# Kernel optimization log

Hardware: AMD Instinct MI355X
Metric: run time of the kernel (lower is better)

## Reference

```python
import jax, jax.numpy as jnp
import numpy as np

B, S, HID = 4, 2048, 2048
NH, NKV, HD = 16, 4, 128  # query heads, kv heads, head_dim


def setup_inputs() -> dict:
    key = jax.random.key(0)
    ks = jax.random.split(key, 7)
    scale = 1.0 / np.sqrt(HID)
    x = jax.random.normal(ks[0], (B, S, HID), dtype=jnp.float32)
    # rope tables (interleaved-pair convention matching rotate_half)
    inv_freq = 1.0 / (1000000.0 ** (np.arange(0, HD, 2, dtype=np.float32) / HD))
    t = np.arange(S, dtype=np.float32)
    freqs = np.outer(t, inv_freq)                      # (S, HD/2)
    emb = np.repeat(freqs, 2, axis=-1)                 # (S, HD) interleaved
    cos = jnp.asarray(np.cos(emb))
    sin = jnp.asarray(np.sin(emb))
    wq = jax.random.normal(ks[1], (HID, NH * HD), dtype=jnp.float32) * scale
    wk = jax.random.normal(ks[2], (HID, NKV * HD), dtype=jnp.float32) * scale
    wv = jax.random.normal(ks[3], (HID, NKV * HD), dtype=jnp.float32) * scale
    wo = jax.random.normal(ks[4], (NH * HD, HID), dtype=jnp.float32) * scale
    return {"x": x, "cos": cos, "sin": sin, "wq": wq, "wk": wk, "wv": wv, "wo": wo}


def _rotate_half(u):
    even = u[..., ::2]
    odd = u[..., 1::2]
    return jnp.stack((-odd, even), axis=-1).reshape(u.shape)


def reference(x, cos, sin, wq, wk, wv, wo):
    b, s, _ = x.shape
    rep = NH // NKV
    q = (x @ wq).reshape(b, s, NH, HD)
    k = (x @ wk).reshape(b, s, NKV, HD)
    v = (x @ wv).reshape(b, s, NKV, HD)
    # RoPE: cos/sin (S, HD) -> broadcast over batch and heads (unsqueeze_dim=1)
    c = cos[:s][None, :, None, :]
    sn = sin[:s][None, :, None, :]
    q = q * c + _rotate_half(q) * sn
    k = k * c + _rotate_half(k) * sn
    # GQA: group query heads per kv head; avoid materializing repeated K/V
    q = q.transpose(0, 2, 1, 3).reshape(b, NKV, rep, s, HD)   # (b, kv, rep, s, d)
    k = k.transpose(0, 2, 1, 3)                                # (b, kv, s, d)
    v = v.transpose(0, 2, 1, 3)                                # (b, kv, s, d)
    scores = jnp.einsum("bgrqd,bgkd->bgrqk", q, k) / jnp.sqrt(jnp.float32(HD))
    causal = jnp.tril(jnp.ones((s, s), dtype=bool))
    scores = jnp.where(causal, scores, jnp.finfo(scores.dtype).min)
    probs = jax.nn.softmax(scores, axis=-1)
    out = jnp.einsum("bgrqk,bgkd->bgrqd", probs, v)            # (b, kv, rep, s, d)
    out = out.reshape(b, NH, s, HD).transpose(0, 2, 1, 3).reshape(b, s, NH * HD)
    return out @ wo
```

## Files before the change

### kernel.cpp

```cpp
#include <hip/hip_runtime.h>

#define HIDD 2048
#define SEQ  2048
#define BATCH 4
#define NHQ  16
#define NKVH 4
#define HDIM 128
#define QKVN 3072

typedef unsigned short u16;
typedef unsigned int   u32;
using bf16x8 = __attribute__((ext_vector_type(8))) __bf16;
using u16x8  = __attribute__((ext_vector_type(8))) u16;
using u16x4  = __attribute__((ext_vector_type(4))) u16;
using f32x4  = __attribute__((ext_vector_type(4))) float;

__device__ __forceinline__ float bf2f(u16 v){ u32 u = ((u32)v) << 16; float f; __builtin_memcpy(&f, &u, 4); return f; }
__device__ __forceinline__ u16 f2bf(float f){ u32 u; __builtin_memcpy(&u, &f, 4); u += 0x7fffu + ((u >> 16) & 1u); return (u16)(u >> 16); }

__device__ __forceinline__ void gl_lds16(const void* g, void* l){
  __builtin_amdgcn_global_load_lds((const __attribute__((address_space(1))) void*)g,
                                   (__attribute__((address_space(3))) void*)l, 16, 0, 0);
}


__global__ void cvt_f32_bf16(const float* __restrict__ in, u16* __restrict__ out, int n4){
  int i = blockIdx.x * 256 + threadIdx.x;
  if (i >= n4) return;
  float4 v = ((const float4*)in)[i];
  u16x4 o; o[0] = f2bf(v.x); o[1] = f2bf(v.y); o[2] = f2bf(v.z); o[3] = f2bf(v.w);
  ((u16x4*)out)[i] = o;
}

__global__ void transpose_cvt_f32(const float* __restrict__ in, u16* __restrict__ out, int R, int C){
  __shared__ float t[32][33];
  int c0 = blockIdx.x * 32, r0 = blockIdx.y * 32;
  int tx = threadIdx.x, ty = threadIdx.y;
  #pragma unroll
  for (int i = 0; i < 4; i++)
    t[ty + 8*i][tx] = in[(size_t)(r0 + ty + 8*i) * C + c0 + tx];
  __syncthreads();
  #pragma unroll
  for (int i = 0; i < 4; i++)
    out[(size_t)(c0 + ty + 8*i) * R + r0 + tx] = f2bf(t[tx][ty + 8*i]);
}

__global__ void transpose_v(const u16* __restrict__ V, u16* __restrict__ Vt, int ld, int voff){
  __shared__ u16 t[32][33];
  int bg = blockIdx.z;
  int b = bg >> 2, g = bg & 3;
  const u16* in = V + (size_t)b * SEQ * ld + voff + g * HDIM;
  u16* out = Vt + (size_t)bg * HDIM * SEQ;
  int c0 = blockIdx.x * 32, r0 = blockIdx.y * 32;
  int tx = threadIdx.x, ty = threadIdx.y;
  #pragma unroll
  for (int i = 0; i < 4; i++)
    t[ty + 8*i][tx] = in[(size_t)(r0 + ty + 8*i) * ld + c0 + tx];
  __syncthreads();
  #pragma unroll
  for (int i = 0; i < 4; i++)
    out[(size_t)(c0 + ty + 8*i) * SEQ + r0 + tx] = t[tx][ty + 8*i];
}

__global__ void rope_kernel(u16* __restrict__ X, int ld, int ncl,
                            const float* __restrict__ ct, const float* __restrict__ st,
                            float scale, int n8){
  int i = blockIdx.x * 256 + threadIdx.x;
  if (i >= n8) return;
  int e0 = i * 8;
  int row = e0 >> ncl;
  int col = e0 & ((1 << ncl) - 1);
  int pos = row & (SEQ - 1);
  int dd  = col & (HDIM - 1);
  u16* p = X + (size_t)row * ld + col;
  u16x8 v = *(const u16x8*)p;
  const float* cp = ct + (size_t)pos * HDIM + dd;
  const float* sp = st + (size_t)pos * HDIM + dd;
  float f[8];
  #pragma unroll
  for (int j = 0; j < 8; j++) f[j] = bf2f(v[j]);
  u16x8 o;
  #pragma unroll
  for (int j = 0; j < 8; j += 2){
    float c = cp[j], s = sp[j];
    float e = f[j], od = f[j+1];
    o[j]   = f2bf((e * c - od * s) * scale);
    o[j+1] = f2bf((od * c + e * s) * scale);
  }
  *(u16x8*)p = o;
}

template<int OUT_BF16>
__global__ __launch_bounds__(256) void gemm_bt(const u16* __restrict__ A, const u16* __restrict__ Bt,
                                               void* __restrict__ Cv, int M, int N, int K){
  __shared__ __align__(16) u16 As[128*32];
  __shared__ __align__(16) u16 Bs[128*32];
  const int tid = threadIdx.x;
  const int wid = tid >> 6, lane = tid & 63;
  const int lr = lane & 15, lk = lane >> 4;
  const int m0 = blockIdx.y * 128, n0 = blockIdx.x * 128;
  const int wr = (wid >> 1) * 64, wc = (wid & 1) * 64;

  f32x4 acc[4][4];
  #pragma unroll
  for (int m = 0; m < 4; m++)
    #pragma unroll
    for (int n = 0; n < 4; n++) acc[m][n] = f32x4{0.f,0.f,0.f,0.f};

  const int srow = lane >> 2;
  const int swz  = ((lane & 3) * 8) ^ ((srow & 3) * 8);
  const u16* Ag = A  + (size_t)(m0 + wid*32 + srow) * K + swz;
  const u16* Bg = Bt + (size_t)(n0 + wid*32 + srow) * K + swz;
  u16* Asl = As + wid * 1024;
  u16* Bsl = Bs + wid * 1024;
  const int rsw = (lr & 3) * 8;

  for (int k0 = 0; k0 < K; k0 += 32){
    gl_lds16(Ag + k0,          Asl);
    gl_lds16(Ag + k0 + 16*K,   Asl + 512);
    gl_lds16(Bg + k0,          Bsl);
    gl_lds16(Bg + k0 + 16*K,   Bsl + 512);
    __syncthreads();
    bf16x8 a[4], b[4];
    #pragma unroll
    for (int m = 0; m < 4; m++) a[m] = *(const bf16x8*)&As[(wr + m*16 + lr)*32 + ((lk*8) ^ rsw)];
    #pragma unroll
    for (int n = 0; n < 4; n++) b[n] = *(const bf16x8*)&Bs[(wc + n*16 + lr)*32 + ((lk*8) ^ rsw)];
    #pragma unroll
    for (int m = 0; m < 4; m++)
      #pragma unroll
      for (int n = 0; n < 4; n++)
        acc[m][n] = __builtin_amdgcn_mfma_f32_16x16x32_bf16(a[m], b[n], acc[m][n], 0, 0, 0);
    __syncthreads();
  }
  #pragma unroll
  for (int m = 0; m < 4; m++)
    #pragma unroll
    for (int n = 0; n < 4; n++)
      #pragma unroll
      for (int i = 0; i < 4; i++){
        int gr = m0 + wr + m*16 + lk*4 + i;
        int gc = n0 + wc + n*16 + lr;
        float v = acc[m][n][i];
        if (OUT_BF16) ((u16*)Cv)[(size_t)gr * N + gc] = f2bf(v);
        else          ((float*)Cv)[(size_t)gr * N + gc] = v;
      }
}

__global__ __launch_bounds__(256) void attn_kernel(const u16* __restrict__ QKV, const u16* __restrict__ Vt,
                                                   u16* __restrict__ O){
  const int qt = (gridDim.x - 1) - blockIdx.x;
  const int h = blockIdx.y, b = blockIdx.z;
  const int g = h >> 2;
  const int tid = threadIdx.x;
  const int wid = tid >> 6, lane = tid & 63;
  const int lr = lane & 15, lk = lane >> 4;
  const int q0 = qt * 128;
  const int q0w = q0 + wid * 32;

  __shared__ __align__(16) u16 Ks[2][64*128];
  __shared__ __align__(16) u16 Vs[2][128*64];
  __shared__ __align__(16) u16 Ps[4][16*72];
  u16* Pw = &Ps[wid][0];

  bf16x8 qf[2][4];
  #pragma unroll
  for (int qh = 0; qh < 2; qh++){
    const u16* qp = QKV + (size_t)(b*SEQ + q0w + qh*16 + lr) * QKVN + h*HDIM + lk*8;
    #pragma unroll
    for (int c = 0; c < 4; c++) qf[qh][c] = *(const bf16x8*)(qp + c*32);
  }

  const int klr = lane >> 4, kj = lane & 15;
  const int vlr = lane >> 3, vj = lane & 7;
  const u16* Kst[4]; const u16* Vst[4];
  {
    const u16* Kbase = QKV + (size_t)b * SEQ * QKVN + HIDD + g*HDIM;
    const u16* Vbase = Vt + (size_t)(b*NKVH + g) * HDIM * SEQ;
    #pragma unroll
    for (int iw = 0; iw < 4; iw++){
      int kcb = wid*4 + iw;
      int r   = kcb*4 + klr;
      Kst[iw] = Kbase + (size_t)r * QKVN + ((kj ^ (r & 7)) << 3);
      int d   = kcb*8 + vlr;
      Vst[iw] = Vbase + (size_t)d * SEQ + ((vj ^ (d & 7)) << 3);
    }
  }

  f32x4 oacc[2][8];
  #pragma unroll
  for (int qh = 0; qh < 2; qh++)
    #pragma unroll
    for (int f = 0; f < 8; f++) oacc[qh][f] = f32x4{0.f,0.f,0.f,0.f};
  float m_i[2] = {-1e30f, -1e30f}, l_i[2] = {0.f, 0.f};

  const int nt = 2 * (qt + 1);
  int cur = 0;
  #pragma unroll
  for (int iw = 0; iw < 4; iw++){
    int kcb = wid*4 + iw;
    gl_lds16(Kst[iw], &Ks[0][kcb << 9]);
    gl_lds16(Vst[iw], &Vs[0][kcb << 9]);
    Kst[iw] += 64 * QKVN;
    Vst[iw] += 64;
  }

  for (int t = 0; t < nt; ++t){
    __syncthreads();
    if (t + 1 < nt){
      #pragma unroll
      for (int iw = 0; iw < 4; iw++){
        int kcb = wid*4 + iw;
        gl_lds16(Kst[iw], &Ks[cur ^ 1][kcb << 9]);
        gl_lds16(Vst[iw], &Vs[cur ^ 1][kcb << 9]);
        Kst[iw] += 64 * QKVN;
        Vst[iw] += 64;
      }
    }
    const int kv0 = t * 64;
    if (kv0 <= q0w + 31){
      f32x4 sf[2][4];
      #pragma unroll
      for (int n = 0; n < 4; n++){
        bf16x8 kf[4];
        #pragma unroll
        for (int c = 0; c < 4; c++)
          kf[c] = *(const bf16x8*)&Ks[cur][(n*16 + lr)*128 + (((c*4 + lk) ^ (lr & 7)) << 3)];
        #pragma unroll
        for (int qh = 0; qh < 2; qh++){
          f32x4 a = f32x4{0.f,0.f,0.f,0.f};
          #pragma unroll
          for (int c = 0; c < 4; c++)
            a = __builtin_amdgcn_mfma_f32_16x16x32_bf16(kf[c], qf[qh][c], a, 0, 0, 0);
          sf[qh][n] = a;
        }
      }
      if (kv0 + 63 > q0w){
        #pragma unroll
        for (int qh = 0; qh < 2; qh++)
          #pragma unroll
          for (int n = 0; n < 4; n++)
            #pragma unroll
            for (int i = 0; i < 4; i++){
              int kvg = kv0 + n*16 + lk*4 + i;
              int qg  = q0w + qh*16 + lr;
              if (kvg > qg) sf[qh][n][i] = -1e30f;
            }
      }
      #pragma unroll
      for (int qh = 0; qh < 2; qh++){
        float rm = sf[qh][0][0];
        #pragma unroll
        for (int n = 0; n < 4; n++)
          #pragma unroll
          for (int i = 0; i < 4; i++) rm = fmaxf(rm, sf[qh][n][i]);
        rm = fmaxf(rm, __shfl_xor(rm, 16));
        rm = fmaxf(rm, __shfl_xor(rm, 32));

        if (!__all(rm <= m_i[qh] + 11.5f)){
          float mn = fmaxf(m_i[qh], rm);
          float cf = exp2f(m_i[qh] - mn);
          m_i[qh] = mn; l_i[qh] *= cf;
          float cfq[4];
          #pragma unroll
          for (int i = 0; i < 4; i++) cfq[i] = __shfl(cf, lk*4 + i);
          #pragma unroll
          for (int f = 0; f < 8; f++)
            #pragma unroll
            for (int i = 0; i < 4; i++) oacc[qh][f][i] *= cfq[i];
        }
        float rs = 0.f;
        #pragma unroll
        for (int n = 0; n < 4; n++){
          u16x4 pp;
          #pragma unroll
          for (int i = 0; i < 4; i++){
            float pv = exp2f(sf[qh][n][i] - m_i[qh]);
            rs += pv;
            pp[i] = f2bf(pv);
          }
          *(u16x4*)&Pw[lr*72 + n*16 + lk*4] = pp;
        }
        rs += __shfl_xor(rs, 16);
        rs += __shfl_xor(rs, 32);
        l_i[qh] += rs;

        #pragma unroll
        for (int kc = 0; kc < 2; kc++){
          bf16x8 pf = *(const bf16x8*)&Pw[lr*72 + kc*32 + lk*8];
          #pragma unroll
          for (int f = 0; f < 8; f++){
            bf16x8 vf = *(const bf16x8*)&Vs[cur][(f*16 + lr)*64 + (((kc*4 + lk) ^ (lr & 7)) << 3)];
            oacc[qh][f] = __builtin_amdgcn_mfma_f32_16x16x32_bf16(pf, vf, oacc[qh][f], 0, 0, 0);
          }
        }
      }
    }
    cur ^= 1;
  }
  #pragma unroll
  for (int qh = 0; qh < 2; qh++){
    float linv[4];
    #pragma unroll
    for (int i = 0; i < 4; i++) linv[i] = 1.0f / __shfl(l_i[qh], lk*4 + i);
    #pragma unroll
    for (int f = 0; f < 8; f++)
      #pragma unroll
      for (int i = 0; i < 4; i++){
        int qr = q0w + qh*16 + lk*4 + i;
        O[(size_t)(b*SEQ + qr) * (NHQ*HDIM) + h*HDIM + f*16 + lr] = f2bf(oacc[qh][f][i] * linv[i]);
      }
  }
}


extern "C" void kernel_launch(void* const* d_in, const int* in_sizes, int n_in,
                              void* d_out, int out_size, void* d_ws, size_t ws_size,
                              hipStream_t stream){
  const float* x    = (const float*)d_in[0];
  const float* cosb = (const float*)d_in[1];
  const float* sinb = (const float*)d_in[2];
  const float* wq   = (const float*)d_in[3];
  const float* wk   = (const float*)d_in[4];
  const float* wv   = (const float*)d_in[5];
  const float* wo   = (const float*)d_in[6];
  float* out = (float*)d_out;

  char* ws = (char*)d_ws;
  u16* XB    = (u16*)(ws);
  u16* WQKVT = (u16*)(ws + 33554432);
  u16* WOT   = (u16*)(ws + 46137344);
  u16* QKV   = (u16*)(ws + 54525952);
  u16* VT    = (u16*)(ws + 104857600);

  dim3 tb(32, 8);
  cvt_f32_bf16<<<(BATCH*SEQ*HIDD/4 + 255)/256, 256, 0, stream>>>(x, XB, BATCH*SEQ*HIDD/4);
  transpose_cvt_f32<<<dim3(HIDD/32, HIDD/32), tb, 0, stream>>>(wq, WQKVT, HIDD, NHQ*HDIM);
  transpose_cvt_f32<<<dim3((NKVH*HDIM)/32, HIDD/32), tb, 0, stream>>>(wk, WQKVT + (size_t)2048*2048, HIDD, NKVH*HDIM);
  transpose_cvt_f32<<<dim3((NKVH*HDIM)/32, HIDD/32), tb, 0, stream>>>(wv, WQKVT + (size_t)2560*2048, HIDD, NKVH*HDIM);
  transpose_cvt_f32<<<dim3(HIDD/32, HIDD/32), tb, 0, stream>>>(wo, WOT, NHQ*HDIM, HIDD);
  gemm_bt<1><<<dim3(QKVN/128, BATCH*SEQ/128), 256, 0, stream>>>(XB, WQKVT, QKV, BATCH*SEQ, QKVN, HIDD);
  rope_kernel<<<(BATCH*SEQ*2048/8)/256, 256, 0, stream>>>(QKV, QKVN, 11, cosb, sinb, 0.12753165651003169f, BATCH*SEQ*2048/8);
  rope_kernel<<<(BATCH*SEQ*512/8)/256, 256, 0, stream>>>(QKV + HIDD, QKVN, 9, cosb, sinb, 1.0f, BATCH*SEQ*512/8);
  transpose_v<<<dim3(HDIM/32, SEQ/32, BATCH*NKVH), tb, 0, stream>>>(QKV, VT, QKVN, 2560);
  attn_kernel<<<dim3(SEQ/128, NHQ, BATCH), 256, 0, stream>>>(QKV, VT, XB);
  gemm_bt<0><<<dim3(HIDD/128, BATCH*SEQ/128), 256, 0, stream>>>(XB, WOT, out, BATCH*SEQ, HIDD, NHQ*HDIM);
}
```

Baseline: 761.5 us.

## Load K/V directly from global in attention, drop LDS staging and block syncs

The attention kernel no longer stages K and V tiles in shared memory with double buffering and __syncthreads. Each wave now loads its K and V fragments straight from global memory into registers, computes a per-wave causal tile count, and masks only on the last tile. The grid is flattened to 1D and remapped so that blocks sharing a KV group land on the same XCD, which should improve L2 reuse of K/V. The trade-off is that K/V reuse across the four waves now depends on L2/cache instead of LDS, with more global load traffic and higher register pressure.

```diff
diff --git a/kernel.cpp b/kernel.cpp
--- a/kernel.cpp
+++ b/kernel.cpp
@@ -149,19 +149,21 @@
 
 __global__ __launch_bounds__(256) void attn_kernel(const u16* __restrict__ QKV, const u16* __restrict__ Vt,
                                                    u16* __restrict__ O){
-  const int qt = (gridDim.x - 1) - blockIdx.x;
-  const int h = blockIdx.y, b = blockIdx.z;
-  const int g = h >> 2;
+  const int F = blockIdx.x;
+  const int xcd = F & 7, slot = F >> 3;
+  const int gi  = xcd + 8 * (slot >> 6);
+  const int j   = slot & 63;
+  const int b = gi >> 2, g = gi & 3;
+  const int h = g * 4 + (j >> 4);
+  const int qt = 15 - (j & 15);
   const int tid = threadIdx.x;
   const int wid = tid >> 6, lane = tid & 63;
   const int lr = lane & 15, lk = lane >> 4;
-  const int q0 = qt * 128;
-  const int q0w = q0 + wid * 32;
-
-  __shared__ __align__(16) u16 Ks[2][64*128];
-  __shared__ __align__(16) u16 Vs[2][128*64];
-  __shared__ __align__(16) u16 Ps[4][16*72];
-  u16* Pw = &Ps[wid][0];
+  const int q0w = qt * 128 + wid * 32;
+
+  __shared__ __align__(16) u16 Ps[4][2][16*72];
+  u16* Pw0 = &Ps[wid][0][0];
+  u16* Pw1 = &Ps[wid][1][0];
 
   bf16x8 qf[2][4];
   #pragma unroll
@@ -171,21 +173,8 @@
     for (int c = 0; c < 4; c++) qf[qh][c] = *(const bf16x8*)(qp + c*32);
   }
 
-  const int klr = lane >> 4, kj = lane & 15;
-  const int vlr = lane >> 3, vj = lane & 7;
-  const u16* Kst[4]; const u16* Vst[4];
-  {
-    const u16* Kbase = QKV + (size_t)b * SEQ * QKVN + HIDD + g*HDIM;
-    const u16* Vbase = Vt + (size_t)(b*NKVH + g) * HDIM * SEQ;
-    #pragma unroll
-    for (int iw = 0; iw < 4; iw++){
-      int kcb = wid*4 + iw;
-      int r   = kcb*4 + klr;
-      Kst[iw] = Kbase + (size_t)r * QKVN + ((kj ^ (r & 7)) << 3);
-      int d   = kcb*8 + vlr;
-      Vst[iw] = Vbase + (size_t)d * SEQ + ((vj ^ (d & 7)) << 3);
-    }
-  }
+  const u16* Kl = QKV + (size_t)b * SEQ * QKVN + HIDD + g*HDIM + (size_t)lr * QKVN + lk*8;
+  const u16* Vl = Vt + (size_t)(b*NKVH + g) * HDIM * SEQ + (size_t)lr * SEQ + lk*8;
 
   f32x4 oacc[2][8];
   #pragma unroll
@@ -194,110 +183,97 @@
     for (int f = 0; f < 8; f++) oacc[qh][f] = f32x4{0.f,0.f,0.f,0.f};
   float m_i[2] = {-1e30f, -1e30f}, l_i[2] = {0.f, 0.f};
 
-  const int nt = 2 * (qt + 1);
-  int cur = 0;
-  #pragma unroll
-  for (int iw = 0; iw < 4; iw++){
-    int kcb = wid*4 + iw;
-    gl_lds16(Kst[iw], &Ks[0][kcb << 9]);
-    gl_lds16(Vst[iw], &Vs[0][kcb << 9]);
-    Kst[iw] += 64 * QKVN;
-    Vst[iw] += 64;
-  }
-
-  for (int t = 0; t < nt; ++t){
-    __syncthreads();
-    if (t + 1 < nt){
-      #pragma unroll
-      for (int iw = 0; iw < 4; iw++){
-        int kcb = wid*4 + iw;
-        gl_lds16(Kst[iw], &Ks[cur ^ 1][kcb << 9]);
-        gl_lds16(Vst[iw], &Vs[cur ^ 1][kcb << 9]);
-        Kst[iw] += 64 * QKVN;
-        Vst[iw] += 64;
-      }
-    }
-    const int kv0 = t * 64;
-    if (kv0 <= q0w + 31){
-      f32x4 sf[2][4];
-      #pragma unroll
-      for (int n = 0; n < 4; n++){
-        bf16x8 kf[4];
+  const int nt = ((q0w + 31) >> 6) + 1;
+  for (int t = 0; t < nt; ++t, Kl += 64*QKVN, Vl += 64){
+    bf16x8 kf[4][4];
+    #pragma unroll
+    for (int n = 0; n < 4; n++)
+      #pragma unroll
+      for (int c = 0; c < 4; c++)
+        kf[n][c] = *(const bf16x8*)(Kl + n*16*QKVN + c*32);
+
+    f32x4 sf[2][4];
+    #pragma unroll
+    for (int n = 0; n < 4; n++)
+      #pragma unroll
+      for (int qh = 0; qh < 2; qh++){
+        f32x4 a = f32x4{0.f,0.f,0.f,0.f};
         #pragma unroll
         for (int c = 0; c < 4; c++)
-          kf[c] = *(const bf16x8*)&Ks[cur][(n*16 + lr)*128 + (((c*4 + lk) ^ (lr & 7)) << 3)];
-        #pragma unroll
-        for (int qh = 0; qh < 2; qh++){
-          f32x4 a = f32x4{0.f,0.f,0.f,0.f};
-          #pragma unroll
-          for (int c = 0; c < 4; c++)
-            a = __builtin_amdgcn_mfma_f32_16x16x32_bf16(kf[c], qf[qh][c], a, 0, 0, 0);
-          sf[qh][n] = a;
-        }
-      }
-      if (kv0 + 63 > q0w){
-        #pragma unroll
-        for (int qh = 0; qh < 2; qh++)
-          #pragma unroll
-          for (int n = 0; n < 4; n++)
-            #pragma unroll
-            for (int i = 0; i < 4; i++){
-              int kvg = kv0 + n*16 + lk*4 + i;
-              int qg  = q0w + qh*16 + lr;
-              if (kvg > qg) sf[qh][n][i] = -1e30f;
-            }
-      }
-      #pragma unroll
-      for (int qh = 0; qh < 2; qh++){
-        float rm = sf[qh][0][0];
+          a = __builtin_amdgcn_mfma_f32_16x16x32_bf16(kf[n][c], qf[qh][c], a, 0, 0, 0);
+        sf[qh][n] = a;
+      }
+
+    if (t == nt - 1){
+      const int kv0 = t * 64;
+      #pragma unroll
+      for (int qh = 0; qh < 2; qh++)
         #pragma unroll
         for (int n = 0; n < 4; n++)
           #pragma unroll
-          for (int i = 0; i < 4; i++) rm = fmaxf(rm, sf[qh][n][i]);
-        rm = fmaxf(rm, __shfl_xor(rm, 16));
-        rm = fmaxf(rm, __shfl_xor(rm, 32));
-
-        if (!__all(rm <= m_i[qh] + 11.5f)){
-          float mn = fmaxf(m_i[qh], rm);
-          float cf = exp2f(m_i[qh] - mn);
-          m_i[qh] = mn; l_i[qh] *= cf;
-          float cfq[4];
+          for (int i = 0; i < 4; i++){
+            int kvg = kv0 + n*16 + lk*4 + i;
+            int qg  = q0w + qh*16 + lr;
+            if (kvg > qg) sf[qh][n][i] = -1e30f;
+          }
+    }
+
+    #pragma unroll
+    for (int qh = 0; qh < 2; qh++){
+      u16* Pw = qh ? Pw1 : Pw0;
+      float rm = sf[qh][0][0];
+      #pragma unroll
+      for (int n = 0; n < 4; n++)
+        #pragma unroll
+        for (int i = 0; i < 4; i++) rm = fmaxf(rm, sf[qh][n][i]);
+      rm = fmaxf(rm, __shfl_xor(rm, 16));
+      rm = fmaxf(rm, __shfl_xor(rm, 32));
+
+      if (!__all(rm <= m_i[qh] + 11.5f)){
+        float mn = fmaxf(m_i[qh], rm);
+        float cf = exp2f(m_i[qh] - mn);
+        m_i[qh] = mn; l_i[qh] *= cf;
+        float cfq[4];
+        #pragma unroll
+        for (int i = 0; i < 4; i++) cfq[i] = __shfl(cf, lk*4 + i);
+        #pragma unroll
+        for (int f = 0; f < 8; f++)
           #pragma unroll
-          for (int i = 0; i < 4; i++) cfq[i] = __shfl(cf, lk*4 + i);
-          #pragma unroll
-          for (int f = 0; f < 8; f++)
-            #pragma unroll
-            for (int i = 0; i < 4; i++) oacc[qh][f][i] *= cfq[i];
+          for (int i = 0; i < 4; i++) oacc[qh][f][i] *= cfq[i];
+      }
+      float rs = 0.f;
+      #pragma unroll
+      for (int n = 0; n < 4; n++){
+        u16x4 pp;
+        #pragma unroll
+        for (int i = 0; i < 4; i++){
+          float pv = exp2f(sf[qh][n][i] - m_i[qh]);
+          rs += pv;
+          pp[i] = f2bf(pv);
         }
-        float rs = 0.f;
-        #pragma unroll
-        for (int n = 0; n < 4; n++){
-          u16x4 pp;
-          #pragma unroll
-          for (int i = 0; i < 4; i++){
-            float pv = exp2f(sf[qh][n][i] - m_i[qh]);
-            rs += pv;
-            pp[i] = f2bf(pv);
-          }
-          *(u16x4*)&Pw[lr*72 + n*16 + lk*4] = pp;
-        }
-        rs += __shfl_xor(rs, 16);
-        rs += __shfl_xor(rs, 32);
-        l_i[qh] += rs;
-
-        #pragma unroll
-        for (int kc = 0; kc < 2; kc++){
-          bf16x8 pf = *(const bf16x8*)&Pw[lr*72 + kc*32 + lk*8];
-          #pragma unroll
-          for (int f = 0; f < 8; f++){
-            bf16x8 vf = *(const bf16x8*)&Vs[cur][(f*16 + lr)*64 + (((kc*4 + lk) ^ (lr & 7)) << 3)];
-            oacc[qh][f] = __builtin_amdgcn_mfma_f32_16x16x32_bf16(pf, vf, oacc[qh][f], 0, 0, 0);
-          }
-        }
-      }
+        *(u16x4*)&Pw[lr*72 + n*16 + lk*4] = pp;
+      }
+      rs += __shfl_xor(rs, 16);
+      rs += __shfl_xor(rs, 32);
+      l_i[qh] += rs;
     }
-    cur ^= 1;
-  }
+
+    #pragma unroll
+    for (int kc = 0; kc < 2; kc++){
+      bf16x8 vf[8];
+      #pragma unroll
+      for (int f = 0; f < 8; f++)
+        vf[f] = *(const bf16x8*)(Vl + f*16*SEQ + kc*32);
+      bf16x8 pf0 = *(const bf16x8*)&Pw0[lr*72 + kc*32 + lk*8];
+      bf16x8 pf1 = *(const bf16x8*)&Pw1[lr*72 + kc*32 + lk*8];
+      #pragma unroll
+      for (int f = 0; f < 8; f++){
+        oacc[0][f] = __builtin_amdgcn_mfma_f32_16x16x32_bf16(pf0, vf[f], oacc[0][f], 0, 0, 0);
+        oacc[1][f] = __builtin_amdgcn_mfma_f32_16x16x32_bf16(pf1, vf[f], oacc[1][f], 0, 0, 0);
+      }
+    }
+  }
+
   #pragma unroll
   for (int qh = 0; qh < 2; qh++){
     float linv[4];
@@ -343,6 +319,6 @@
   rope_kernel<<<(BATCH*SEQ*2048/8)/256, 256, 0, stream>>>(QKV, QKVN, 11, cosb, sinb, 0.12753165651003169f, BATCH*SEQ*2048/8);
   rope_kernel<<<(BATCH*SEQ*512/8)/256, 256, 0, stream>>>(QKV + HIDD, QKVN, 9, cosb, sinb, 1.0f, BATCH*SEQ*512/8);
   transpose_v<<<dim3(HDIM/32, SEQ/32, BATCH*NKVH), tb, 0, stream>>>(QKV, VT, QKVN, 2560);
-  attn_kernel<<<dim3(SEQ/128, NHQ, BATCH), 256, 0, stream>>>(QKV, VT, XB);
+  attn_kernel<<<dim3(SEQ/128 * NHQ * BATCH), 256, 0, stream>>>(QKV, VT, XB);
   gemm_bt<0><<<dim3(HIDD/128, BATCH*SEQ/128), 256, 0, stream>>>(XB, WOT, out, BATCH*SEQ, HIDD, NHQ*HDIM);
 }
```

Result: slower. 862.8 us (+13.3%).

## Pair complementary causal query tiles per attention block for load balance

Applied to the files above, without the earlier changes.

Each attention workgroup now processes two query tiles in sequence, tile 15-p and tile p, so every block does the same total amount of causal work. The grid shrinks from 16 to 8 tiles along x, giving 512 uniform blocks instead of 1024 blocks of very uneven length. The goal is to remove the tail imbalance of causal attention. In exchange there are fewer blocks to hide latency, and each block runs the pipeline prologue and epilogue twice.

```diff
diff --git a/kernel.cpp b/kernel.cpp
--- a/kernel.cpp
+++ b/kernel.cpp
@@ -149,31 +149,21 @@
 
 __global__ __launch_bounds__(256) void attn_kernel(const u16* __restrict__ QKV, const u16* __restrict__ Vt,
                                                    u16* __restrict__ O){
-  const int qt = (gridDim.x - 1) - blockIdx.x;
+  const int p = blockIdx.x;
   const int h = blockIdx.y, b = blockIdx.z;
   const int g = h >> 2;
   const int tid = threadIdx.x;
   const int wid = tid >> 6, lane = tid & 63;
   const int lr = lane & 15, lk = lane >> 4;
-  const int q0 = qt * 128;
-  const int q0w = q0 + wid * 32;
 
   __shared__ __align__(16) u16 Ks[2][64*128];
   __shared__ __align__(16) u16 Vs[2][128*64];
   __shared__ __align__(16) u16 Ps[4][16*72];
   u16* Pw = &Ps[wid][0];
 
-  bf16x8 qf[2][4];
-  #pragma unroll
-  for (int qh = 0; qh < 2; qh++){
-    const u16* qp = QKV + (size_t)(b*SEQ + q0w + qh*16 + lr) * QKVN + h*HDIM + lk*8;
-    #pragma unroll
-    for (int c = 0; c < 4; c++) qf[qh][c] = *(const bf16x8*)(qp + c*32);
-  }
-
   const int klr = lane >> 4, kj = lane & 15;
   const int vlr = lane >> 3, vj = lane & 7;
-  const u16* Kst[4]; const u16* Vst[4];
+  const u16* Kst0[4]; const u16* Vst0[4];
   {
     const u16* Kbase = QKV + (size_t)b * SEQ * QKVN + HIDD + g*HDIM;
     const u16* Vbase = Vt + (size_t)(b*NKVH + g) * HDIM * SEQ;
@@ -181,135 +171,154 @@
     for (int iw = 0; iw < 4; iw++){
       int kcb = wid*4 + iw;
       int r   = kcb*4 + klr;
-      Kst[iw] = Kbase + (size_t)r * QKVN + ((kj ^ (r & 7)) << 3);
+      Kst0[iw] = Kbase + (size_t)r * QKVN + ((kj ^ (r & 7)) << 3);
       int d   = kcb*8 + vlr;
-      Vst[iw] = Vbase + (size_t)d * SEQ + ((vj ^ (d & 7)) << 3);
+      Vst0[iw] = Vbase + (size_t)d * SEQ + ((vj ^ (d & 7)) << 3);
     }
   }
 
-  f32x4 oacc[2][8];
-  #pragma unroll
-  for (int qh = 0; qh < 2; qh++)
-    #pragma unroll
-    for (int f = 0; f < 8; f++) oacc[qh][f] = f32x4{0.f,0.f,0.f,0.f};
-  float m_i[2] = {-1e30f, -1e30f}, l_i[2] = {0.f, 0.f};
-
-  const int nt = 2 * (qt + 1);
-  int cur = 0;
-  #pragma unroll
-  for (int iw = 0; iw < 4; iw++){
-    int kcb = wid*4 + iw;
-    gl_lds16(Kst[iw], &Ks[0][kcb << 9]);
-    gl_lds16(Vst[iw], &Vs[0][kcb << 9]);
-    Kst[iw] += 64 * QKVN;
-    Vst[iw] += 64;
-  }
-
-  for (int t = 0; t < nt; ++t){
+  for (int seg = 0; seg < 2; ++seg){
+    const int qt  = seg ? p : (15 - p);
+    const int q0w = qt * 128 + wid * 32;
+
+    bf16x8 qf[2][4];
+    #pragma unroll
+    for (int qh = 0; qh < 2; qh++){
+      const u16* qp = QKV + (size_t)(b*SEQ + q0w + qh*16 + lr) * QKVN + h*HDIM + lk*8;
+      #pragma unroll
+      for (int c = 0; c < 4; c++) qf[qh][c] = *(const bf16x8*)(qp + c*32);
+    }
+
+    const u16* Kl[4]; const u16* Vl[4];
+    #pragma unroll
+    for (int iw = 0; iw < 4; iw++){ Kl[iw] = Kst0[iw]; Vl[iw] = Vst0[iw]; }
+
+    f32x4 oacc[2][8];
+    #pragma unroll
+    for (int qh = 0; qh < 2; qh++)
+      #pragma unroll
+      for (int f = 0; f < 8; f++) oacc[qh][f] = f32x4{0.f,0.f,0.f,0.f};
+    float m_i[2] = {-1e30f, -1e30f}, l_i[2] = {0.f, 0.f};
+
     __syncthreads();
-    if (t + 1 < nt){
-      #pragma unroll
-      for (int iw = 0; iw < 4; iw++){
-        int kcb = wid*4 + iw;
-        gl_lds16(Kst[iw], &Ks[cur ^ 1][kcb << 9]);
-        gl_lds16(Vst[iw], &Vs[cur ^ 1][kcb << 9]);
-        Kst[iw] += 64 * QKVN;
-        Vst[iw] += 64;
+
+    const int nt = 2 * (qt + 1);
+    int cur = 0;
+    #pragma unroll
+    for (int iw = 0; iw < 4; iw++){
+      int kcb = wid*4 + iw;
+      gl_lds16(Kl[iw], &Ks[0][kcb << 9]);
+      gl_lds16(Vl[iw], &Vs[0][kcb << 9]);
+      Kl[iw] += 64 * QKVN;
+      Vl[iw] += 64;
+    }
+
+    for (int t = 0; t < nt; ++t){
+      __syncthreads();
+      if (t + 1 < nt){
+        #pragma unroll
+        for (int iw = 0; iw < 4; iw++){
+          int kcb = wid*4 + iw;
+          gl_lds16(Kl[iw], &Ks[cur ^ 1][kcb << 9]);
+          gl_lds16(Vl[iw], &Vs[cur ^ 1][kcb << 9]);
+          Kl[iw] += 64 * QKVN;
+          Vl[iw] += 64;
+        }
       }
-    }
-    const int kv0 = t * 64;
-    if (kv0 <= q0w + 31){
-      f32x4 sf[2][4];
-      #pragma unroll
-      for (int n = 0; n < 4; n++){
-        bf16x8 kf[4];
+      const int kv0 = t * 64;
+      if (kv0 <= q0w + 31){
+        f32x4 sf[2][4];
         #pragma unroll
-        for (int c = 0; c < 4; c++)
-          kf[c] = *(const bf16x8*)&Ks[cur][(n*16 + lr)*128 + (((c*4 + lk) ^ (lr & 7)) << 3)];
+        for (int n = 0; n < 4; n++){
+          bf16x8 kf[4];
+          #pragma unroll
+          for (int c = 0; c < 4; c++)
+            kf[c] = *(const bf16x8*)&Ks[cur][(n*16 + lr)*128 + (((c*4 + lk) ^ (lr & 7)) << 3)];
+          #pragma unroll
+          for (int qh = 0; qh < 2; qh++){
+            f32x4 a = f32x4{0.f,0.f,0.f,0.f};
+            #pragma unroll
+            for (int c = 0; c < 4; c++)
+              a = __builtin_amdgcn_mfma_f32_16x16x32_bf16(kf[c], qf[qh][c], a, 0, 0, 0);
+            sf[qh][n] = a;
+          }
+        }
+        if (kv0 + 63 > q0w){
+          #pragma unroll
+          for (int qh = 0; qh < 2; qh++)
+            #pragma unroll
+            for (int n = 0; n < 4; n++)
+              #pragma unroll
+              for (int i = 0; i < 4; i++){
+                int kvg = kv0 + n*16 + lk*4 + i;
+                int qg  = q0w + qh*16 + lr;
+                if (kvg > qg) sf[qh][n][i] = -1e30f;
+              }
+        }
         #pragma unroll
         for (int qh = 0; qh < 2; qh++){
-          f32x4 a = f32x4{0.f,0.f,0.f,0.f};
-          #pragma unroll
-          for (int c = 0; c < 4; c++)
-            a = __builtin_amdgcn_mfma_f32_16x16x32_bf16(kf[c], qf[qh][c], a, 0, 0, 0);
-          sf[qh][n] = a;
+          float rm = sf[qh][0][0];
+          #pragma unroll
+          for (int n = 0; n < 4; n++)
+            #pragma unroll
+            for (int i = 0; i < 4; i++) rm = fmaxf(rm, sf[qh][n][i]);
+          rm = fmaxf(rm, __shfl_xor(rm, 16));
+          rm = fmaxf(rm, __shfl_xor(rm, 32));
+
+          if (!__all(rm <= m_i[qh] + 11.5f)){
+            float mn = fmaxf(m_i[qh], rm);
+            float cf = exp2f(m_i[qh] - mn);
+            m_i[qh] = mn; l_i[qh] *= cf;
+            float cfq[4];
+            #pragma unroll
+            for (int i = 0; i < 4; i++) cfq[i] = __shfl(cf, lk*4 + i);
+            #pragma unroll
+            for (int f = 0; f < 8; f++)
+              #pragma unroll
+              for (int i = 0; i < 4; i++) oacc[qh][f][i] *= cfq[i];
+          }
+          float rs = 0.f;
+          #pragma unroll
+          for (int n = 0; n < 4; n++){
+            u16x4 pp;
+            #pragma unroll
+            for (int i = 0; i < 4; i++){
+              float pv = exp2f(sf[qh][n][i] - m_i[qh]);
+              rs += pv;
+              pp[i] = f2bf(pv);
+            }
+            *(u16x4*)&Pw[lr*72 + n*16 + lk*4] = pp;
+          }
+          rs += __shfl_xor(rs, 16);
+          rs += __shfl_xor(rs, 32);
+          l_i[qh] += rs;
+
+          #pragma unroll
+          for (int kc = 0; kc < 2; kc++){
+            bf16x8 pf = *(const bf16x8*)&Pw[lr*72 + kc*32 + lk*8];
+            #pragma unroll
+            for (int f = 0; f < 8; f++){
+              bf16x8 vf = *(const bf16x8*)&Vs[cur][(f*16 + lr)*64 + (((kc*4 + lk) ^ (lr & 7)) << 3)];
+              oacc[qh][f] = __builtin_amdgcn_mfma_f32_16x16x32_bf16(pf, vf, oacc[qh][f], 0, 0, 0);
+            }
+          }
         }
       }
-      if (kv0 + 63 > q0w){
+      cur ^= 1;
+    }
+    #pragma unroll
+    for (int qh = 0; qh < 2; qh++){
+      float linv[4];
+      #pragma unroll
+      for (int i = 0; i < 4; i++) linv[i] = 1.0f / __shfl(l_i[qh], lk*4 + i);
+      #pragma unroll
+      for (int f = 0; f < 8; f++)
         #pragma unroll
-        for (int qh = 0; qh < 2; qh++)
-          #pragma unroll
-          for (int n = 0; n < 4; n++)
-            #pragma unroll
-            for (int i = 0; i < 4; i++){
-              int kvg = kv0 + n*16 + lk*4 + i;
-              int qg  = q0w + qh*16 + lr;
-              if (kvg > qg) sf[qh][n][i] = -1e30f;
-            }
-      }
-      #pragma unroll
-      for (int qh = 0; qh < 2; qh++){
-        float rm = sf[qh][0][0];
-        #pragma unroll
-        for (int n = 0; n < 4; n++)
-          #pragma unroll
-          for (int i = 0; i < 4; i++) rm = fmaxf(rm, sf[qh][n][i]);
-        rm = fmaxf(rm, __shfl_xor(rm, 16));
-        rm = fmaxf(rm, __shfl_xor(rm, 32));
-
-        if (!__all(rm <= m_i[qh] + 11.5f)){
-          float mn = fmaxf(m_i[qh], rm);
-          float cf = exp2f(m_i[qh] - mn);
-          m_i[qh] = mn; l_i[qh] *= cf;
-          float cfq[4];
-          #pragma unroll
-          for (int i = 0; i < 4; i++) cfq[i] = __shfl(cf, lk*4 + i);
-          #pragma unroll
-          for (int f = 0; f < 8; f++)
-            #pragma unroll
-            for (int i = 0; i < 4; i++) oacc[qh][f][i] *= cfq[i];
-        }
-        float rs = 0.f;
-        #pragma unroll
-        for (int n = 0; n < 4; n++){
-          u16x4 pp;
-          #pragma unroll
-          for (int i = 0; i < 4; i++){
-            float pv = exp2f(sf[qh][n][i] - m_i[qh]);
-            rs += pv;
-            pp[i] = f2bf(pv);
-          }
-          *(u16x4*)&Pw[lr*72 + n*16 + lk*4] = pp;
-        }
-        rs += __shfl_xor(rs, 16);
-        rs += __shfl_xor(rs, 32);
-        l_i[qh] += rs;
-
-        #pragma unroll
-        for (int kc = 0; kc < 2; kc++){
-          bf16x8 pf = *(const bf16x8*)&Pw[lr*72 + kc*32 + lk*8];
-          #pragma unroll
-          for (int f = 0; f < 8; f++){
-            bf16x8 vf = *(const bf16x8*)&Vs[cur][(f*16 + lr)*64 + (((kc*4 + lk) ^ (lr & 7)) << 3)];
-            oacc[qh][f] = __builtin_amdgcn_mfma_f32_16x16x32_bf16(pf, vf, oacc[qh][f], 0, 0, 0);
-          }
-        }
-      }
-    }
-    cur ^= 1;
-  }
-  #pragma unroll
-  for (int qh = 0; qh < 2; qh++){
-    float linv[4];
-    #pragma unroll
-    for (int i = 0; i < 4; i++) linv[i] = 1.0f / __shfl(l_i[qh], lk*4 + i);
-    #pragma unroll
-    for (int f = 0; f < 8; f++)
-      #pragma unroll
-      for (int i = 0; i < 4; i++){
-        int qr = q0w + qh*16 + lk*4 + i;
-        O[(size_t)(b*SEQ + qr) * (NHQ*HDIM) + h*HDIM + f*16 + lr] = f2bf(oacc[qh][f][i] * linv[i]);
-      }
+        for (int i = 0; i < 4; i++){
+          int qr = q0w + qh*16 + lk*4 + i;
+          O[(size_t)(b*SEQ + qr) * (NHQ*HDIM) + h*HDIM + f*16 + lr] = f2bf(oacc[qh][f][i] * linv[i]);
+        }
+    }
   }
 }
 
@@ -343,6 +352,6 @@
   rope_kernel<<<(BATCH*SEQ*2048/8)/256, 256, 0, stream>>>(QKV, QKVN, 11, cosb, sinb, 0.12753165651003169f, BATCH*SEQ*2048/8);
   rope_kernel<<<(BATCH*SEQ*512/8)/256, 256, 0, stream>>>(QKV + HIDD, QKVN, 9, cosb, sinb, 1.0f, BATCH*SEQ*512/8);
   transpose_v<<<dim3(HDIM/32, SEQ/32, BATCH*NKVH), tb, 0, stream>>>(QKV, VT, QKVN, 2560);
-  attn_kernel<<<dim3(SEQ/128, NHQ, BATCH), 256, 0, stream>>>(QKV, VT, XB);
+  attn_kernel<<<dim3(8, NHQ, BATCH), 256, 0, stream>>>(QKV, VT, XB);
   gemm_bt<0><<<dim3(HIDD/128, BATCH*SEQ/128), 256, 0, stream>>>(XB, WOT, out, BATCH*SEQ, HIDD, NHQ*HDIM);
 }
```

Measured after the change: 618.3 us. 18.8% less time.
